# Kernel tuning notes

Measured on AMD Instinct MI355X. Metric: run time of the kernel, lower is better.

Reference implementation:

```python
import jax, jax.numpy as jnp
import numpy as np
import math

B, L, D, H = 4, 4096, 1024, 16
DH = D // H  # 64


def setup_inputs() -> dict:
    key = jax.random.key(0)
    ks = jax.random.split(key, 11)
    s = 1.0 / math.sqrt(D)
    return {
        "query": jax.random.normal(ks[0], (B, L, D), jnp.float32),
        "key_": jax.random.normal(ks[1], (B, L, D), jnp.float32),
        "value": jax.random.normal(ks[2], (B, L, D), jnp.float32),
        "Wq": jax.random.normal(ks[3], (D, D), jnp.float32) * s,
        "bq": jax.random.normal(ks[4], (D,), jnp.float32) * s,
        "Wk": jax.random.normal(ks[5], (D, D), jnp.float32) * s,
        "bk": jax.random.normal(ks[6], (D,), jnp.float32) * s,
        "Wv": jax.random.normal(ks[7], (D, D), jnp.float32) * s,
        "bv": jax.random.normal(ks[8], (D,), jnp.float32) * s,
        "Wo": jax.random.normal(ks[9], (D, D), jnp.float32) * s,
        "bo": jax.random.normal(ks[10], (D,), jnp.float32) * s,
    }


def reference(query, key_, value, Wq, bq, Wk, bk, Wv, bv, Wo, bo):
    # Linear projections (torch Linear: x @ W.T + b)
    q = (query @ Wq.T + bq).reshape(B, L, DH, H)   # heads in LAST dim (faithful quirk)
    k = (key_ @ Wk.T + bk).reshape(B, L, DH, H)
    v = (value @ Wv.T + bv).reshape(B, L, DH, H)
    # per-(batch, position) matmul: [B,L,DH,H] @ [B,L,H,DH] -> [B,L,DH,DH]
    scores = jnp.einsum('blih,bljh->blij', q, k) * jnp.asarray(math.sqrt(D), q.dtype)
    attn = jax.nn.softmax(scores, axis=-1)
    out = jnp.einsum('blij,bljh->blih', attn, v).reshape(B, L, D)
    return out @ Wo.T + bo
```

## Files before the change

kernel.cpp:

```cpp
#include <hip/hip_runtime.h>

typedef float    f32x4 __attribute__((ext_vector_type(4)));
typedef _Float16 h16x8 __attribute__((ext_vector_type(8)));
typedef _Float16 h16x4 __attribute__((ext_vector_type(4)));

#define DEV __device__ __forceinline__

DEV void async_load16(const void* g, void* l) {
  __builtin_amdgcn_global_load_lds((const __attribute__((address_space(1))) void*)g,
                                   (__attribute__((address_space(3))) void*)l,
                                   16, 0, 0);
}

template <int AMODE, bool OF32>
DEV void gemm_core(const void* Av, const _Float16* __restrict__ Bw,
                   const float* __restrict__ bias, void* Cv) {
  constexpr int K = 1024, N = 1024;
  __shared__ __align__(16) _Float16 As[128 * 32];
  __shared__ __align__(16) _Float16 Bs[128 * 32];

  const int tid  = threadIdx.x;
  const int lane = tid & 63;
  const int w    = tid >> 6;
  const int d    = blockIdx.x;
  const int bm   = (d & 7) | ((d >> 6) << 3);
  const int bn   = (d >> 3) & 7;
  const int rowbase = bm << 7;
  const int colbase = bn << 7;
  const int wm = w >> 1, wn = w & 1;
  const int m16 = lane & 15, q = lane >> 4;
  const int brow = lane >> 2;
  const int bcol = (lane & 3) * 8;

  f32x4 acc[4][4];
#pragma unroll
  for (int nt = 0; nt < 4; ++nt) {
    const float bv = bias[colbase + wn * 64 + nt * 16 + m16];
#pragma unroll
    for (int mt = 0; mt < 4; ++mt) acc[mt][nt] = {bv, bv, bv, bv};
  }

  for (int ki = 0; ki < 32; ++ki) {
    const int k0 = ki * 32;
    if constexpr (AMODE == 0) {
      const _Float16* A = (const _Float16*)Av;
#pragma unroll
      for (int t = 0; t < 2; ++t)
        async_load16(A + (size_t)(rowbase + (w * 2 + t) * 16 + brow) * K + k0 + bcol,
                     &As[(w * 2 + t) * 512]);
    } else {
      const float* A = (const float*)Av;
#pragma unroll
      for (int i = 0; i < 4; ++i) {
        const int f = tid + i * 256;
        const int r = f >> 3, c4 = f & 7;
        const float4 v = *(const float4*)(A + (size_t)(rowbase + r) * K + k0 + c4 * 4);
        h16x4 o = {(_Float16)v.x, (_Float16)v.y, (_Float16)v.z, (_Float16)v.w};
        *(h16x4*)&As[r * 32 + c4 * 4] = o;
      }
    }
#pragma unroll
    for (int t = 0; t < 2; ++t)
      async_load16(Bw + (size_t)(colbase + (w * 2 + t) * 16 + brow) * K + k0 + bcol,
                   &Bs[(w * 2 + t) * 512]);
    __syncthreads();

    h16x8 af[4], bfr[4];
#pragma unroll
    for (int mt = 0; mt < 4; ++mt)
      af[mt] = *(const h16x8*)&As[(wm * 64 + mt * 16 + m16) * 32 + q * 8];
#pragma unroll
    for (int nt = 0; nt < 4; ++nt)
      bfr[nt] = *(const h16x8*)&Bs[(wn * 64 + nt * 16 + m16) * 32 + q * 8];
#pragma unroll
    for (int mt = 0; mt < 4; ++mt)
#pragma unroll
      for (int nt = 0; nt < 4; ++nt)
        acc[mt][nt] = __builtin_amdgcn_mfma_f32_16x16x32_f16(af[mt], bfr[nt], acc[mt][nt], 0, 0, 0);
    __syncthreads();
  }

#pragma unroll
  for (int mt = 0; mt < 4; ++mt) {
#pragma unroll
    for (int nt = 0; nt < 4; ++nt) {
      const int col = colbase + wn * 64 + nt * 16 + m16;
#pragma unroll
      for (int r = 0; r < 4; ++r) {
        const int row = rowbase + wm * 64 + mt * 16 + q * 4 + r;
        if constexpr (OF32)
          ((float*)Cv)[(size_t)row * N + col] = acc[mt][nt][r];
        else
          ((_Float16*)Cv)[(size_t)row * N + col] = (_Float16)acc[mt][nt][r];
      }
    }
  }
}

__global__ __launch_bounds__(256) void k_cvt_w(const float* __restrict__ Wq,
                                               const float* __restrict__ Wk,
                                               const float* __restrict__ Wv,
                                               const float* __restrict__ Wo,
                                               _Float16* __restrict__ dst) {
  const float* src;
  switch (blockIdx.y) {
    case 0: src = Wq; break;
    case 1: src = Wk; break;
    case 2: src = Wv; break;
    default: src = Wo; break;
  }
  _Float16* d = dst + (size_t)blockIdx.y * (1024 * 1024);
  const int idx = blockIdx.x * 256 + threadIdx.x;
  const float4 v = ((const float4*)src)[idx];
  h16x4 o = {(_Float16)v.x, (_Float16)v.y, (_Float16)v.z, (_Float16)v.w};
  ((h16x4*)d)[idx] = o;
}

__global__ __launch_bounds__(256) void k_cvt_a(const float* __restrict__ q,
                                               const float* __restrict__ k,
                                               const float* __restrict__ v,
                                               _Float16* __restrict__ dst) {
  const float* src = (blockIdx.y == 0) ? q : (blockIdx.y == 1) ? k : v;
  _Float16* d = dst + (size_t)blockIdx.y * ((size_t)16384 * 1024);
  const size_t idx = (size_t)blockIdx.x * 256 + threadIdx.x;
  const float4 vv = ((const float4*)src)[idx];
  h16x4 o = {(_Float16)vv.x, (_Float16)vv.y, (_Float16)vv.z, (_Float16)vv.w};
  ((h16x4*)d)[idx] = o;
}

__global__ __launch_bounds__(256) void k_gemm_qkv_f16(const _Float16* __restrict__ xf,
                                                      const _Float16* __restrict__ Wf,
                                                      const float* __restrict__ bq,
                                                      const float* __restrict__ bk,
                                                      const float* __restrict__ bv,
                                                      _Float16* __restrict__ proj) {
  constexpr size_t MW = 1024 * 1024, MA = (size_t)16384 * 1024;
  const int y = blockIdx.y;
  const float* bias = (y == 0) ? bq : (y == 1) ? bk : bv;
  gemm_core<0, false>(xf + y * MA, Wf + y * MW, bias, proj + y * MA);
}

__global__ __launch_bounds__(256) void k_gemm_qkv_f32(const float* __restrict__ q,
                                                      const float* __restrict__ k,
                                                      const float* __restrict__ v,
                                                      const _Float16* __restrict__ Wf,
                                                      const float* __restrict__ bq,
                                                      const float* __restrict__ bk,
                                                      const float* __restrict__ bv,
                                                      _Float16* __restrict__ proj) {
  constexpr size_t MW = 1024 * 1024, MA = (size_t)16384 * 1024;
  const int y = blockIdx.y;
  const float* A    = (y == 0) ? q  : (y == 1) ? k  : v;
  const float* bias = (y == 0) ? bq : (y == 1) ? bk : bv;
  gemm_core<1, false>(A, Wf + y * MW, bias, proj + y * MA);
}

__global__ __launch_bounds__(256) void k_gemm_out(const _Float16* __restrict__ ao,
                                                  const _Float16* __restrict__ Wof,
                                                  const float* __restrict__ bo,
                                                  float* __restrict__ C) {
  gemm_core<0, true>(ao, Wof, bo, C);
}

__global__ __launch_bounds__(256) void k_attn(const _Float16* __restrict__ qp,
                                              const _Float16* __restrict__ kp,
                                              const _Float16* __restrict__ vp,
                                              _Float16* __restrict__ op) {
  constexpr int RS2 = 20;
  __shared__ __align__(16) _Float16 vsh[4][64 * RS2];
  const int w    = threadIdx.x >> 6;
  const int lane = threadIdx.x & 63;
  const int g    = lane >> 4;
  const int t    = lane & 15;
  const size_t base = ((size_t)blockIdx.x * 4 + w) * 1024;

  {
    h16x8 v0 = *(const h16x8*)(vp + base + lane * 16);
    h16x8 v1 = *(const h16x8*)(vp + base + lane * 16 + 8);
    _Float16* vr = &vsh[w][lane * RS2];
    h16x4 a0, a1, a2, a3;
#pragma unroll
    for (int e = 0; e < 4; ++e) {
      a0[e] = v0[e]; a1[e] = v0[4 + e]; a2[e] = v1[e]; a3[e] = v1[4 + e];
    }
    *(h16x4*)(vr + 0)  = a0;
    *(h16x4*)(vr + 4)  = a1;
    *(h16x4*)(vr + 8)  = a2;
    *(h16x4*)(vr + 12) = a3;
  }

  h16x4 kA[4], qB[4];
#pragma unroll
  for (int jt = 0; jt < 4; ++jt) {
    kA[jt] = *(const h16x4*)(kp + base + (jt * 16 + t) * 16 + g * 4);
    qB[jt] = *(const h16x4*)(qp + base + (jt * 16 + t) * 16 + g * 4);
  }

  f32x4 st[4][4];
#pragma unroll
  for (int jt = 0; jt < 4; ++jt)
#pragma unroll
    for (int nt = 0; nt < 4; ++nt)
      st[jt][nt] = __builtin_amdgcn_mfma_f32_16x16x16f16(
          kA[jt], qB[nt], (f32x4){0.f, 0.f, 0.f, 0.f}, 0, 0, 0);

  h16x4 pb[4][4];
  float inv[4];
#pragma unroll
  for (int nt = 0; nt < 4; ++nt) {
    float mx = -3.0e38f;
#pragma unroll
    for (int jt = 0; jt < 4; ++jt)
#pragma unroll
      for (int r = 0; r < 4; ++r) mx = fmaxf(mx, st[jt][nt][r]);
    mx = fmaxf(mx, __shfl_xor(mx, 16));
    mx = fmaxf(mx, __shfl_xor(mx, 32));
    float sum = 0.f;
#pragma unroll
    for (int jt = 0; jt < 4; ++jt) {
#pragma unroll
      for (int r = 0; r < 4; ++r) {
        const float p = __expf((st[jt][nt][r] - mx) * 32.0f);
        sum += p;
        pb[jt][nt][r] = (_Float16)p;
      }
    }
    sum += __shfl_xor(sum, 16);
    sum += __shfl_xor(sum, 32);
    inv[nt] = 1.0f / sum;
  }

  h16x4 vA[4];
#pragma unroll
  for (int kt = 0; kt < 4; ++kt)
#pragma unroll
    for (int e = 0; e < 4; ++e)
      vA[kt][e] = vsh[w][(kt * 16 + g * 4 + e) * RS2 + t];

#pragma unroll
  for (int it = 0; it < 4; ++it) {
    f32x4 ot = {0.f, 0.f, 0.f, 0.f};
#pragma unroll
    for (int kt = 0; kt < 4; ++kt)
      ot = __builtin_amdgcn_mfma_f32_16x16x16f16(vA[kt], pb[kt][it], ot, 0, 0, 0);
    h16x4 o;
#pragma unroll
    for (int r = 0; r < 4; ++r) o[r] = (_Float16)(ot[r] * inv[it]);
    *(h16x4*)(op + base + (it * 16 + t) * 16 + g * 4) = o;
  }
}

extern "C" void kernel_launch(void* const* d_in, const int* in_sizes, int n_in,
                              void* d_out, int out_size, void* d_ws, size_t ws_size,
                              hipStream_t stream) {
  const float* query = (const float*)d_in[0];
  const float* key_  = (const float*)d_in[1];
  const float* value = (const float*)d_in[2];
  const float* Wq    = (const float*)d_in[3];
  const float* bq    = (const float*)d_in[4];
  const float* Wk    = (const float*)d_in[5];
  const float* bk    = (const float*)d_in[6];
  const float* Wv    = (const float*)d_in[7];
  const float* bv    = (const float*)d_in[8];
  const float* Wo    = (const float*)d_in[9];
  const float* bo    = (const float*)d_in[10];

  constexpr size_t MW = 1024 * 1024;
  constexpr size_t MA = (size_t)16384 * 1024;

  _Float16* Wf = (_Float16*)d_ws;
  const size_t needA = (4 * MW + 6 * MA) * sizeof(_Float16);

  k_cvt_w<<<dim3(1024, 4), 256, 0, stream>>>(Wq, Wk, Wv, Wo, Wf);

  if (ws_size >= needA) {
    _Float16* xf   = Wf + 4 * MW;
    _Float16* proj = xf + 3 * MA;
    _Float16* ao   = xf;
    k_cvt_a<<<dim3(16384, 3), 256, 0, stream>>>(query, key_, value, xf);
    k_gemm_qkv_f16<<<dim3(1024, 3), 256, 0, stream>>>(xf, Wf, bq, bk, bv, proj);
    k_attn<<<4096, 256, 0, stream>>>(proj, proj + MA, proj + 2 * MA, ao);
    k_gemm_out<<<1024, 256, 0, stream>>>(ao, Wf + 3 * MW, bo, (float*)d_out);
  } else {
    _Float16* proj = Wf + 4 * MW;
    _Float16* ao   = proj + 3 * MA;
    k_gemm_qkv_f32<<<dim3(1024, 3), 256, 0, stream>>>(query, key_, value, Wf,
                                                      bq, bk, bv, proj);
    k_attn<<<4096, 256, 0, stream>>>(proj, proj + MA, proj + 2 * MA, ao);
    k_gemm_out<<<1024, 256, 0, stream>>>(ao, Wf + 3 * MW, bo, (float*)d_out);
  }
}
```

Baseline: 444.9 us.

## Replace 128x128 GEMMs with 256x256-tile, 8-wave pipelined MFMA GEMM

```diff
diff --git a/kernel.cpp b/kernel.cpp
--- a/kernel.cpp
+++ b/kernel.cpp
@@ -10,6 +10,141 @@
   __builtin_amdgcn_global_load_lds((const __attribute__((address_space(1))) void*)g,
                                    (__attribute__((address_space(3))) void*)l,
                                    16, 0, 0);
+}
+
+template <bool OF32>
+DEV void gemm256_core(const _Float16* __restrict__ A, const _Float16* __restrict__ Bw,
+                      const float* __restrict__ bias, void* Cv, int bm, int bn) {
+  constexpr int N = 1024;
+  __shared__ __align__(16) _Float16 lds[2 * 2 * 2 * 8192];
+  char* ldsb = (char*)lds;
+
+  const int tid  = threadIdx.x;
+  const int lane = tid & 63;
+  const int w    = tid >> 6;
+  const int wm   = w >> 2, wn = w & 3;
+  const int m16  = lane & 15, q = lane >> 4;
+  const int rowbase = bm << 8;
+  const int colbase = bn << 8;
+
+  const int sr0 = (w * 2 + 0) * 16 + (lane >> 2);
+  const int sr1 = (w * 2 + 1) * 16 + (lane >> 2);
+  const int ss  = lane & 3;
+  const int sc0 = ((ss ^ ((sr0 ^ (sr0 >> 2)) & 3)) * 8);
+  const int sc1 = ((ss ^ ((sr1 ^ (sr1 >> 2)) & 3)) * 8);
+
+  auto stA = [&](int buf, int kk, int gk) {
+    async_load16(A + (size_t)(rowbase + sr0) * 1024 + gk + kk * 32 + sc0,
+                 ldsb + buf * 65536 + kk * 16384 + (w * 2 + 0) * 1024);
+    async_load16(A + (size_t)(rowbase + sr1) * 1024 + gk + kk * 32 + sc1,
+                 ldsb + buf * 65536 + kk * 16384 + (w * 2 + 1) * 1024);
+  };
+  auto stB = [&](int buf, int kk, int gk) {
+    async_load16(Bw + (size_t)(colbase + sr0) * 1024 + gk + kk * 32 + sc0,
+                 ldsb + buf * 65536 + 32768 + kk * 16384 + (w * 2 + 0) * 1024);
+    async_load16(Bw + (size_t)(colbase + sr1) * 1024 + gk + kk * 32 + sc1,
+                 ldsb + buf * 65536 + 32768 + kk * 16384 + (w * 2 + 1) * 1024);
+  };
+
+  int aoff[8], boff[4];
+#pragma unroll
+  for (int mt = 0; mt < 8; ++mt) {
+    const int r = wm * 128 + mt * 16 + m16;
+    aoff[mt] = r * 64 + ((q ^ ((r ^ (r >> 2)) & 3)) * 16);
+  }
+#pragma unroll
+  for (int nt = 0; nt < 4; ++nt) {
+    const int r = wn * 64 + nt * 16 + m16;
+    boff[nt] = r * 64 + ((q ^ ((r ^ (r >> 2)) & 3)) * 16);
+  }
+
+  f32x4 acc[8][4];
+#pragma unroll
+  for (int nt = 0; nt < 4; ++nt) {
+    const float bv = bias[colbase + wn * 64 + nt * 16 + m16];
+#pragma unroll
+    for (int mt = 0; mt < 8; ++mt) acc[mt][nt] = {bv, bv, bv, bv};
+  }
+
+  stA(0, 0, 0); stB(0, 0, 0); stA(0, 1, 0); stB(0, 1, 0);
+  stA(1, 0, 64); stB(1, 0, 64);
+  asm volatile("s_waitcnt vmcnt(4)" ::: "memory");
+  __builtin_amdgcn_s_barrier();
+  __builtin_amdgcn_sched_barrier(0);
+
+  h16x8 bfr[4];
+
+#define PHASE(BUF_, KK_, MH_, STAGE_, VM_)                                      \
+  {                                                                             \
+    const char* pA = ldsb + (BUF_) * 65536 + (KK_) * 16384;                     \
+    const char* pB = pA + 32768;                                                \
+    h16x8 a[4];                                                                 \
+    _Pragma("unroll")                                                           \
+    for (int m_ = 0; m_ < 4; ++m_)                                              \
+      a[m_] = *(const h16x8*)(pA + aoff[(MH_) * 4 + m_]);                       \
+    if ((MH_) == 0) {                                                           \
+      _Pragma("unroll")                                                         \
+      for (int n_ = 0; n_ < 4; ++n_)                                            \
+        bfr[n_] = *(const h16x8*)(pB + boff[n_]);                               \
+    }                                                                           \
+    STAGE_                                                                      \
+    VM_                                                                         \
+    __builtin_amdgcn_s_barrier();                                               \
+    asm volatile("s_waitcnt lgkmcnt(0)" ::: "memory");                          \
+    __builtin_amdgcn_sched_barrier(0);                                          \
+    __builtin_amdgcn_s_setprio(1);                                              \
+    _Pragma("unroll")                                                           \
+    for (int m_ = 0; m_ < 4; ++m_)                                              \
+      _Pragma("unroll")                                                         \
+      for (int n_ = 0; n_ < 4; ++n_)                                            \
+        acc[(MH_) * 4 + m_][n_] = __builtin_amdgcn_mfma_f32_16x16x32_f16(       \
+            a[m_], bfr[n_], acc[(MH_) * 4 + m_][n_], 0, 0, 0);                  \
+    __builtin_amdgcn_s_setprio(0);                                              \
+    __builtin_amdgcn_s_barrier();                                               \
+    __builtin_amdgcn_sched_barrier(0);                                          \
+  }
+
+  for (int i = 0; i < 7; ++i) {
+    const int g1 = (2 * i + 1) * 64, g2 = (2 * i + 2) * 64, g3 = (2 * i + 3) * 64;
+    PHASE(0, 0, 0, { stA(1, 1, g1); stB(1, 1, g1); }, {})
+    PHASE(0, 0, 1, {}, {})
+    PHASE(0, 1, 0, { stA(0, 0, g2); }, {})
+    PHASE(0, 1, 1, { stB(0, 0, g2); },
+          { asm volatile("s_waitcnt vmcnt(4)" ::: "memory"); })
+    PHASE(1, 0, 0, { stA(0, 1, g2); stB(0, 1, g2); }, {})
+    PHASE(1, 0, 1, {}, {})
+    PHASE(1, 1, 0, { stA(1, 0, g3); }, {})
+    PHASE(1, 1, 1, { stB(1, 0, g3); },
+          { asm volatile("s_waitcnt vmcnt(4)" ::: "memory"); })
+  }
+  {
+    const int g1 = 15 * 64;
+    PHASE(0, 0, 0, { stA(1, 1, g1); stB(1, 1, g1); }, {})
+    PHASE(0, 0, 1, {}, {})
+    PHASE(0, 1, 0, {}, {})
+    PHASE(0, 1, 1, {}, { asm volatile("s_waitcnt vmcnt(0)" ::: "memory"); })
+    PHASE(1, 0, 0, {}, {})
+    PHASE(1, 0, 1, {}, {})
+    PHASE(1, 1, 0, {}, {})
+    PHASE(1, 1, 1, {}, {})
+  }
+#undef PHASE
+
+#pragma unroll
+  for (int mt = 0; mt < 8; ++mt) {
+#pragma unroll
+    for (int nt = 0; nt < 4; ++nt) {
+      const int col = colbase + wn * 64 + nt * 16 + m16;
+#pragma unroll
+      for (int r = 0; r < 4; ++r) {
+        const int row = rowbase + wm * 128 + mt * 16 + q * 4 + r;
+        if constexpr (OF32)
+          ((float*)Cv)[(size_t)row * N + col] = acc[mt][nt][r];
+        else
+          ((_Float16*)Cv)[(size_t)row * N + col] = (_Float16)acc[mt][nt][r];
+      }
+    }
+  }
 }
 
 template <int AMODE, bool OF32>
@@ -128,16 +263,29 @@
   ((h16x4*)d)[idx] = o;
 }
 
-__global__ __launch_bounds__(256) void k_gemm_qkv_f16(const _Float16* __restrict__ xf,
-                                                      const _Float16* __restrict__ Wf,
-                                                      const float* __restrict__ bq,
-                                                      const float* __restrict__ bk,
-                                                      const float* __restrict__ bv,
-                                                      _Float16* __restrict__ proj) {
+__global__ __launch_bounds__(512, 2) void k_gemm_qkv_256(const _Float16* __restrict__ xf,
+                                                         const _Float16* __restrict__ Wf,
+                                                         const float* __restrict__ bq,
+                                                         const float* __restrict__ bk,
+                                                         const float* __restrict__ bv,
+                                                         _Float16* __restrict__ proj) {
   constexpr size_t MW = 1024 * 1024, MA = (size_t)16384 * 1024;
   const int y = blockIdx.y;
   const float* bias = (y == 0) ? bq : (y == 1) ? bk : bv;
-  gemm_core<0, false>(xf + y * MA, Wf + y * MW, bias, proj + y * MA);
+  const int d  = blockIdx.x;
+  const int bm = (d & 7) + ((d >> 5) << 3);
+  const int bn = (d >> 3) & 3;
+  gemm256_core<false>(xf + y * MA, Wf + y * MW, bias, proj + y * MA, bm, bn);
+}
+
+__global__ __launch_bounds__(512, 2) void k_gemm_out_256(const _Float16* __restrict__ ao,
+                                                         const _Float16* __restrict__ Wof,
+                                                         const float* __restrict__ bo,
+                                                         float* __restrict__ C) {
+  const int d  = blockIdx.x;
+  const int bm = (d & 7) + ((d >> 5) << 3);
+  const int bn = (d >> 3) & 3;
+  gemm256_core<true>(ao, Wof, bo, C, bm, bn);
 }
 
 __global__ __launch_bounds__(256) void k_gemm_qkv_f32(const float* __restrict__ q,
@@ -153,13 +301,6 @@
   const float* A    = (y == 0) ? q  : (y == 1) ? k  : v;
   const float* bias = (y == 0) ? bq : (y == 1) ? bk : bv;
   gemm_core<1, false>(A, Wf + y * MW, bias, proj + y * MA);
-}
-
-__global__ __launch_bounds__(256) void k_gemm_out(const _Float16* __restrict__ ao,
-                                                  const _Float16* __restrict__ Wof,
-                                                  const float* __restrict__ bo,
-                                                  float* __restrict__ C) {
-  gemm_core<0, true>(ao, Wof, bo, C);
 }
 
 __global__ __launch_bounds__(256) void k_attn(const _Float16* __restrict__ qp,
@@ -278,15 +419,15 @@
     _Float16* proj = xf + 3 * MA;
     _Float16* ao   = xf;
     k_cvt_a<<<dim3(16384, 3), 256, 0, stream>>>(query, key_, value, xf);
-    k_gemm_qkv_f16<<<dim3(1024, 3), 256, 0, stream>>>(xf, Wf, bq, bk, bv, proj);
+    k_gemm_qkv_256<<<dim3(256, 3), 512, 0, stream>>>(xf, Wf, bq, bk, bv, proj);
     k_attn<<<4096, 256, 0, stream>>>(proj, proj + MA, proj + 2 * MA, ao);
-    k_gemm_out<<<1024, 256, 0, stream>>>(ao, Wf + 3 * MW, bo, (float*)d_out);
+    k_gemm_out_256<<<256, 512, 0, stream>>>(ao, Wf + 3 * MW, bo, (float*)d_out);
   } else {
     _Float16* proj = Wf + 4 * MW;
     _Float16* ao   = proj + 3 * MA;
     k_gemm_qkv_f32<<<dim3(1024, 3), 256, 0, stream>>>(query, key_, value, Wf,
                                                       bq, bk, bv, proj);
     k_attn<<<4096, 256, 0, stream>>>(proj, proj + MA, proj + 2 * MA, ao);
-    k_gemm_out<<<1024, 256, 0, stream>>>(ao, Wf + 3 * MW, bo, (float*)d_out);
-  }
-}
+    k_gemm_out_256<<<256, 512, 0, stream>>>(ao, Wf + 3 * MW, bo, (float*)d_out);
+  }
+}
```

Measured after the change: 419.8 us. 1.06x faster.
